# Optimization experiments

Measured on AMD Instinct MI355X. Metric: run time of the kernel, lower is better.

Reference implementation:

```python
import jax, jax.numpy as jnp
import numpy as np

SEQ = 4096
D_EMB = 2048
D_HEAD = 128
SCALE = 0.02


def setup_inputs() -> dict:
    key = jax.random.key(0)
    kx, kq, kk, kv, ko = jax.random.split(key, 5)
    x = jax.random.normal(kx, (SEQ, D_EMB), dtype=jnp.float32)
    W_Q = jax.random.normal(kq, (D_EMB, D_EMB), dtype=jnp.float32) * SCALE
    W_K = jax.random.normal(kk, (D_EMB, D_EMB), dtype=jnp.float32) * SCALE
    W_V = jax.random.normal(kv, (D_EMB, D_EMB), dtype=jnp.float32) * SCALE
    W_O = jax.random.normal(ko, (D_EMB, D_EMB), dtype=jnp.float32) * SCALE
    b_Q = jnp.zeros((D_EMB,), dtype=jnp.float32)
    b_K = jnp.zeros((D_EMB,), dtype=jnp.float32)
    b_V = jnp.zeros((D_EMB,), dtype=jnp.float32)
    b_O = jnp.zeros((D_EMB,), dtype=jnp.float32)
    return {"x": x, "W_Q": W_Q, "W_K": W_K, "W_V": W_V, "W_O": W_O,
            "b_Q": b_Q, "b_K": b_K, "b_V": b_V, "b_O": b_O, "d_head": D_HEAD}


def reference(x, W_Q, W_K, W_V, W_O, b_Q, b_K, b_V, b_O, d_head):
    # x: [S, D]
    q = x @ W_Q + b_Q  # [S, D]
    k = x @ W_K + b_K
    v = x @ W_V + b_V
    scores = (q @ k.T) / jnp.sqrt(jnp.float32(d_head))  # [S, S]
    seq = scores.shape[0]
    causal = jnp.tril(jnp.ones((seq, seq), dtype=bool))
    scores = jnp.where(causal, scores, -jnp.inf)
    weights = jax.nn.softmax(scores, axis=-1)  # [S, S]
    attn_out = weights @ v  # [S, D]
    return attn_out @ W_O + b_O
```

## Files before the change

### kernel.cpp

```cpp
#include <hip/hip_runtime.h>
#include <hip/hip_fp16.h>

typedef _Float16 f16;
typedef _Float16 f16x8 __attribute__((ext_vector_type(8)));
typedef _Float16 f16x4 __attribute__((ext_vector_type(4)));
typedef float    f32x4 __attribute__((ext_vector_type(4)));

#define SEQ      4096
#define DEMB     2048
#define SCALE_QK 0.08838834764831845f

#define GAS __attribute__((address_space(1)))
#define LAS __attribute__((address_space(3)))

__device__ __forceinline__ void load_lds16(const f16* g, f16* l) {
    __builtin_amdgcn_global_load_lds((const GAS void*)g, (LAS void*)l, 16, 0, 0);
}

__device__ __forceinline__ f16x8 ldsr(const f16* base, int byteoff) {
    byteoff ^= (byteoff >> 3) & 0x70;
    return *(const f16x8*)((const char*)base + byteoff);
}

__device__ __forceinline__ void stage_half(const f16* __restrict__ src, int ldk,
                                           f16* ldsdst, int tid) {
#pragma unroll
    for (int s = 0; s < 2; ++s) {
        const int o   = s * 8192 + tid * 16;
        const int osw = o ^ ((o >> 3) & 0x70);
        load_lds16(src + (size_t)(osw >> 7) * ldk + ((osw & 127) >> 1),
                   ldsdst + (s * 8192 + (tid >> 6) * 1024) / 2);
    }
}

template <int MODE>
__device__ __forceinline__ void gemm_core(
        const f16* __restrict__ A, int lda, const f16* __restrict__ BT, int ldb,
        void* __restrict__ outp, int ldo, const float* __restrict__ bias,
        int bm, int bn, int NI, int kt0, float scale, f16* lds, int roff) {
    const int m0 = bm * 256, n0 = bn * 256;

    const int tid  = threadIdx.x;
    const int lane = tid & 63;
    const int wr   = (tid >> 6) >> 2;
    const int wc   = (tid >> 6) & 3;
    const int fr   = lane & 15;
    const int kb   = (lane >> 4) * 16;

    const f16* Abase = A + (size_t)m0 * lda + kt0 * 64;
    const f16* Bbase = BT + (size_t)n0 * ldb + kt0 * 64;

#define STG(buf, isB, half, t) \
    stage_half((isB) ? (Bbase + (size_t)((half) * 128) * ldb + (t) * 64) \
                     : (Abase + (size_t)((half) * 128) * lda + (t) * 64), \
               (isB) ? ldb : lda, \
               lds + (buf) * 32768 + (isB) * 16384 + (half) * 8192, tid)

    f32x4 acc[8][4] = {};
    f16x8 af[8], bf0[4], bf1[4];

#define READ_A(Mh, buf) { \
    const f16* bb = lds + (buf) * 32768; \
    _Pragma("unroll") for (int m = 0; m < 4; ++m) \
    _Pragma("unroll") for (int ks = 0; ks < 2; ++ks) \
        af[m * 2 + ks] = ldsr(bb, ((Mh) * 128 + wr * 64 + m * 16 + fr) * 128 + ks * 64 + kb); }

#define READ_B(Nh, buf, dst) { \
    const f16* bb = lds + (buf) * 32768 + 16384; \
    _Pragma("unroll") for (int n = 0; n < 2; ++n) \
    _Pragma("unroll") for (int ks = 0; ks < 2; ++ks) \
        dst[n * 2 + ks] = ldsr(bb, ((Nh) * 128 + wc * 32 + n * 16 + fr) * 128 + ks * 64 + kb); }

#define MFMA_PH(Mh, Nh, bfx) { \
    __builtin_amdgcn_s_setprio(1); \
    _Pragma("unroll") for (int m = 0; m < 4; ++m) \
    _Pragma("unroll") for (int n = 0; n < 2; ++n) \
    _Pragma("unroll") for (int ks = 0; ks < 2; ++ks) \
        acc[(Mh) * 4 + m][(Nh) * 2 + n] = __builtin_amdgcn_mfma_f32_16x16x32_f16( \
            af[m * 2 + ks], bfx[n * 2 + ks], acc[(Mh) * 4 + m][(Nh) * 2 + n], 0, 0, 0); \
    __builtin_amdgcn_s_setprio(0); }

#define BAR   asm volatile("s_barrier" ::: "memory")
#define VM6   asm volatile("s_waitcnt vmcnt(6)" ::: "memory")
#define VM0   asm volatile("s_waitcnt vmcnt(0)" ::: "memory")

    STG(0, 0, 0, 0); STG(0, 1, 0, 0); STG(0, 1, 1, 0); STG(0, 0, 1, 0);
    STG(1, 0, 0, 1); STG(1, 1, 0, 1); STG(1, 1, 1, 1);
    VM6; BAR;

    for (int i = 0; i < NI; ++i) {
        const int t0 = 2 * i;
        const bool more = (i + 1 < NI);
        READ_A(0, 0); READ_B(0, 0, bf0);
        STG(1, 0, 1, t0 + 1);
        BAR; MFMA_PH(0, 0, bf0); BAR;
        READ_B(1, 0, bf1);
        if (more) STG(0, 0, 0, t0 + 2);
        BAR; MFMA_PH(0, 1, bf1); BAR;
        READ_A(1, 0);
        if (more) STG(0, 1, 0, t0 + 2);
        BAR; MFMA_PH(1, 0, bf0); BAR;
        if (more) { STG(0, 1, 1, t0 + 2); VM6; } else { VM0; }
        BAR; MFMA_PH(1, 1, bf1); BAR;
        READ_A(0, 1); READ_B(0, 1, bf0);
        if (more) STG(0, 0, 1, t0 + 2);
        BAR; MFMA_PH(0, 0, bf0); BAR;
        READ_B(1, 1, bf1);
        if (more) STG(1, 0, 0, t0 + 3);
        BAR; MFMA_PH(0, 1, bf1); BAR;
        READ_A(1, 1);
        if (more) STG(1, 1, 0, t0 + 3);
        BAR; MFMA_PH(1, 0, bf0); BAR;
        if (more) STG(1, 1, 1, t0 + 3);
        VM6;
        BAR; MFMA_PH(1, 1, bf1); BAR;
    }

    const int rq = (lane >> 4) * 4;
#pragma unroll
    for (int mi = 0; mi < 8; ++mi) {
        const int row = m0 + (mi >> 2) * 128 + wr * 64 + (mi & 3) * 16 + rq;
#pragma unroll
        for (int ni = 0; ni < 4; ++ni) {
            const int col = n0 + (ni >> 1) * 128 + wc * 32 + (ni & 1) * 16 + fr;
            if (MODE == 0) {
                f16* o = (f16*)outp;
                const float bv = bias[col];
#pragma unroll
                for (int r = 0; r < 4; ++r)
                    o[(size_t)(row + r) * ldo + col] = (f16)(acc[mi][ni][r] + bv);
            } else if (MODE == 1) {
                f16* o = (f16*)outp;
                f16x4 v;
#pragma unroll
                for (int r = 0; r < 4; ++r) v[r] = (f16)acc[mi][ni][r];
                *(f16x4*)&o[(size_t)col * ldo + row] = v;
            } else if (MODE == 2) {
                float* o = (float*)outp;
                if (bias) {
                    const float bv = bias[col];
#pragma unroll
                    for (int r = 0; r < 4; ++r)
                        o[(size_t)(row + r) * ldo + col] = acc[mi][ni][r] + bv;
                } else {
#pragma unroll
                    for (int r = 0; r < 4; ++r)
                        o[(size_t)(row - roff + r) * ldo + col] = acc[mi][ni][r];
                }
            } else {
                f16* o = (f16*)outp;
#pragma unroll
                for (int r = 0; r < 4; ++r)
                    o[(size_t)(row + r) * ldo + col] = (f16)(acc[mi][ni][r] * scale);
            }
        }
    }
#undef STG
#undef READ_A
#undef READ_B
#undef MFMA_PH
#undef BAR
#undef VM6
#undef VM0
}

__global__ __launch_bounds__(256) void k_prep(
        const float* __restrict__ x, const float* __restrict__ WV,
        const float* __restrict__ WQ, const float* __restrict__ WK,
        const float* __restrict__ WO,
        const float* __restrict__ bQ, const float* __restrict__ bK,
        const float* __restrict__ bO,
        f16* __restrict__ x16, f16* __restrict__ wv16,
        f16* __restrict__ wqkt, f16* __restrict__ wot,
        float* __restrict__ bqk, float* __restrict__ bc) {
    __shared__ f16 tile[64][72];
    const int bid = blockIdx.x;
    if (bid < 12288) {
        const bool isX = bid < 8192;
        const float* src = isX ? x : WV;
        f16* dst = isX ? x16 : wv16;
        const int i = (isX ? bid : bid - 8192) * 1024 + threadIdx.x * 4;
        float4 v = *(const float4*)&src[i];
        f16x4 o; o[0] = (f16)v.x; o[1] = (f16)v.y; o[2] = (f16)v.z; o[3] = (f16)v.w;
        *(f16x4*)&dst[i] = o;
        return;
    }
    if (bid < 12292) {
        const int i = (bid - 12288) * 1024 + threadIdx.x * 4;
        float4 v = (i < 2048) ? *(const float4*)&bQ[i]
                              : *(const float4*)&bK[i - 2048];
        *(float4*)&bqk[i] = v;
        return;
    }
    if (bid < 12294) {
        const int i = (bid - 12292) * 1024 + threadIdx.x * 4;
        *(float4*)&bc[i] = *(const float4*)&bO[i];
        return;
    }
    const int b = bid - 12294;
    const int z = b >> 10;
    const int rem = b & 1023;
    const float* in = z == 0 ? WQ : z == 1 ? WK : WO;
    f16* out = z == 0 ? wqkt : z == 1 ? wqkt + (size_t)DEMB * DEMB : wot;
    const int c0 = (rem & 31) * 64, r0 = (rem >> 5) * 64;
    const int tx = threadIdx.x & 63, ty = threadIdx.x >> 6;
    for (int rr = ty; rr < 64; rr += 4)
        tile[tx][rr] = (f16)in[(size_t)(r0 + rr) * DEMB + c0 + tx];
    __syncthreads();
    for (int cc = ty; cc < 64; cc += 4)
        out[(size_t)(c0 + cc) * DEMB + r0 + tx] = tile[cc][tx];
}

__global__ __launch_bounds__(512, 2)
void k_mix1(const f16* __restrict__ x16, const f16* __restrict__ wqkt,
            f16* __restrict__ qk16, const float* __restrict__ bqk,
            const f16* __restrict__ wv16, const f16* __restrict__ wot,
            f16* __restrict__ wvoT, const float* __restrict__ WO,
            const float* __restrict__ bV, float* __restrict__ bc) {
    __shared__ f16 lds[65536];
    const int bid = blockIdx.x;
    if (bid < 128) {
        gemm_core<0>(x16, DEMB, wqkt, DEMB, qk16, 2 * DEMB, bqk,
                     bid >> 4, bid & 15, 16, 0, 1.f, lds, 0);
    } else if (bid < 192) {
        const int w = bid - 128;
        gemm_core<1>(wv16, DEMB, wot, DEMB, wvoT, DEMB, nullptr,
                     w >> 3, w & 7, 16, 0, 1.f, lds, 0);
    } else {
        const int b  = bid - 192;
        const int j0 = (b & 7) * 256;
        const int i0 = (b >> 3) * 256 + (threadIdx.x >> 8) * 128;
        const int jj = threadIdx.x & 255;
        float acc = 0.f;
        for (int i = i0; i < i0 + 128; ++i)
            acc += bV[i] * WO[(size_t)i * DEMB + j0 + jj];
        atomicAdd(&bc[j0 + jj], acc);
    }
}

__global__ __launch_bounds__(512, 2)
void k_mix2(const f16* __restrict__ x16, const f16* __restrict__ wqkt,
            f16* __restrict__ qk16, const float* __restrict__ bqk,
            const f16* __restrict__ wvoT, f16* __restrict__ vwT) {
    __shared__ f16 lds[65536];
    const int bid = blockIdx.x;
    if (bid < 128) {
        gemm_core<0>(x16, DEMB, wqkt, DEMB, qk16, 2 * DEMB, bqk,
                     8 + (bid >> 4), bid & 15, 16, 0, 1.f, lds, 0);
    } else {
        const int b = bid - 128;
        const int bmv = ((b & 7) << 1) | ((b >> 3) & 1);
        const int bnv = b >> 4;
        gemm_core<1>(x16, DEMB, wvoT, DEMB, vwT, SEQ, nullptr,
                     bmv, bnv, 16, 0, 1.f, lds, 0);
    }
}

__global__ __launch_bounds__(512, 2)
void k_scores(const f16* __restrict__ qk16, f16* __restrict__ sb) {
    __shared__ f16 lds[65536];
    const int l = blockIdx.x;
    const int bid = (l & 7) * 17 + (l >> 3);
    int bm = (int)((sqrtf(8.f * bid + 1.f) - 1.f) * 0.5f);
    while ((bm + 1) * (bm + 2) / 2 <= bid) ++bm;
    while (bm * (bm + 1) / 2 > bid) --bm;
    const int bn = bid - bm * (bm + 1) / 2;
    gemm_core<3>(qk16, 2 * DEMB, qk16 + DEMB, 2 * DEMB, sb, SEQ, nullptr,
                 bm, bn, 16, 0, SCALE_QK, lds, 0);
}

__global__ __launch_bounds__(256) void k_softmax(f16* __restrict__ sb) {
    __shared__ f16 srow[SEQ];
    __shared__ float red[8];
    const int i  = blockIdx.x;
    const int L  = i + 1;
    const int Lp = ((i >> 8) + 1) << 8;
    f16* row = sb + (size_t)i * SEQ;
    const int t = threadIdx.x;

    float mx = -3.0e38f;
    for (int j0 = t * 8; j0 < Lp; j0 += 2048) {
        f16x8 v = *(const f16x8*)&row[j0];
        *(f16x8*)&srow[j0] = v;
#pragma unroll
        for (int u = 0; u < 8; ++u)
            if (j0 + u < L) mx = fmaxf(mx, (float)v[u]);
    }
#pragma unroll
    for (int o = 32; o > 0; o >>= 1) mx = fmaxf(mx, __shfl_xor(mx, o));
    if ((t & 63) == 0) red[t >> 6] = mx;
    __syncthreads();
    mx = fmaxf(fmaxf(red[0], red[1]), fmaxf(red[2], red[3]));

    float sm = 0.f;
    for (int j0 = t * 8; j0 < Lp; j0 += 2048) {
        f16x8 v = *(const f16x8*)&srow[j0];
        f16x8 e;
#pragma unroll
        for (int u = 0; u < 8; ++u) {
            const float ev = (j0 + u < L) ? __expf((float)v[u] - mx) : 0.f;
            sm += ev;
            e[u] = (f16)ev;
        }
        *(f16x8*)&srow[j0] = e;
    }
#pragma unroll
    for (int o = 32; o > 0; o >>= 1) sm += __shfl_xor(sm, o);
    if ((t & 63) == 0) red[4 + (t >> 6)] = sm;
    __syncthreads();
    const float inv = 1.f / (red[4] + red[5] + red[6] + red[7]);

    for (int j0 = t * 8; j0 < Lp; j0 += 2048) {
        f16x8 e = *(const f16x8*)&srow[j0];
        f16x8 wv;
#pragma unroll
        for (int u = 0; u < 8; ++u)
            wv[u] = (f16)((float)e[u] * inv);
        *(f16x8*)&row[j0] = wv;
    }
}

__global__ __launch_bounds__(512, 2)
void k_pvw(const f16* __restrict__ sb, const f16* __restrict__ vwT,
           float* __restrict__ out, const float* __restrict__ bc,
           float* __restrict__ part1, float* __restrict__ part2) {
    __shared__ f16 lds[65536];
    static const short BMt[32]  = {0,1,2,3,4, 5,5, 6,6, 7,7, 8,8, 9,9, 10,10,
                                   11,11,11, 12,12,12, 13,13,13, 14,14,14,
                                   15,15,15};
    static const short KT0t[32] = {0,0,0,0,0, 0,12, 0,14, 0,16, 0,18, 0,20,
                                   0,22, 0,16,32, 0,18,36, 0,20,38, 0,20,40,
                                   0,22,44};
    static const short NIt[32]  = {2,4,6,8,10, 6,6, 7,7, 8,8, 9,9, 10,10,
                                   11,11, 8,8,8, 9,9,8, 10,9,9, 10,10,10,
                                   11,11,10};
    static const short ORDt[32] = {0,0,0,0,0, 0,1, 0,1, 0,1, 0,1, 0,1, 0,1,
                                   0,1,2, 0,1,2, 0,1,2, 0,1,2, 0,1,2};
    const int bn = blockIdx.x, e = blockIdx.y;
    const int bm = BMt[e], kt0 = KT0t[e], ni = NIt[e], ord = ORDt[e];
    float* op = ord == 0 ? out : ord == 1 ? part1 : part2;
    const int roff = ord == 1 ? 1280 : 2816;
    gemm_core<2>(sb, SEQ, vwT, SEQ, op, DEMB, ord == 0 ? bc : nullptr,
                 bm, bn, ni, kt0, 1.f, lds, roff);
}

__global__ __launch_bounds__(256) void k_reduce(
        float* __restrict__ out, const float* __restrict__ part1,
        const float* __restrict__ part2) {
    const int idx = (blockIdx.x * 256 + threadIdx.x) * 4;
    float4 o = *(float4*)&out[(size_t)1280 * DEMB + idx];
    float4 p = *(const float4*)&part1[idx];
    o.x += p.x; o.y += p.y; o.z += p.z; o.w += p.w;
    if (idx >= 1536 * DEMB) {
        float4 q = *(const float4*)&part2[idx - 1536 * DEMB];
        o.x += q.x; o.y += q.y; o.z += q.z; o.w += q.w;
    }
    *(float4*)&out[(size_t)1280 * DEMB + idx] = o;
}

extern "C" void kernel_launch(void* const* d_in, const int* in_sizes, int n_in,
                              void* d_out, int out_size, void* d_ws, size_t ws_size,
                              hipStream_t stream) {
    const float* x  = (const float*)d_in[0];
    const float* WQ = (const float*)d_in[1];
    const float* WK = (const float*)d_in[2];
    const float* WV = (const float*)d_in[3];
    const float* WO = (const float*)d_in[4];
    const float* bQ = (const float*)d_in[5];
    const float* bK = (const float*)d_in[6];
    const float* bV = (const float*)d_in[7];
    const float* bO = (const float*)d_in[8];
    float* out = (float*)d_out;

    char* w = (char*)d_ws;
    f16* qk16 = (f16*)w; w += (size_t)SEQ * 2 * DEMB * 2;
    f16* sb   = (f16*)w; w += (size_t)SEQ * SEQ * 2;
    f16* x16  = (f16*)w; w += (size_t)SEQ * DEMB * 2;
    f16* wqkt = (f16*)w; w += (size_t)2 * DEMB * DEMB * 2;
    f16* wv16 = (f16*)w; w += (size_t)DEMB * DEMB * 2;
    f16* wot  = (f16*)w; w += (size_t)DEMB * DEMB * 2;
    f16* wvoT = (f16*)w; w += (size_t)DEMB * DEMB * 2;
    float* bqk = (float*)w; w += 2 * DEMB * 4;
    float* bc  = (float*)w; w += DEMB * 4 + 4096;
    f16* vwT = wv16;
    float* part1 = (float*)qk16;
    float* part2 = (float*)wqkt;

    k_prep<<<15366, 256, 0, stream>>>(x, WV, WQ, WK, WO, bQ, bK, bO,
                                      x16, wv16, wqkt, wot, bqk, bc);

    k_mix1<<<256, 512, 0, stream>>>(x16, wqkt, qk16, bqk, wv16, wot, wvoT,
                                    WO, bV, bc);

    k_mix2<<<256, 512, 0, stream>>>(x16, wqkt, qk16, bqk, wvoT, vwT);

    k_scores<<<136, 512, 0, stream>>>(qk16, sb);

    k_softmax<<<SEQ, 256, 0, stream>>>(sb);

    k_pvw<<<dim3(8, 32), 512, 0, stream>>>(sb, vwT, out, bc, part1, part2);

    k_reduce<<<5632, 256, 0, stream>>>(out, part1, part2);
}
```

Measured before the change: 278.6 us.

## Merge GEMM MFMA phases into four per iteration and regroup staging loads

Restructures the GEMM main loop from eight barrier-separated MFMA phases into four larger phases. Each phase now covers both N-halves, reading both B fragments up front. Staging loads are grouped three at a time and the vmcnt wait threshold drops from 6 to 3 to match. The aim is to halve the barrier count and give each MFMA burst more work, at the cost of more live B-fragment registers and less interleaving of global loads with compute.

```diff
diff --git a/kernel.cpp b/kernel.cpp
--- a/kernel.cpp
+++ b/kernel.cpp
@@ -71,49 +71,51 @@
     _Pragma("unroll") for (int ks = 0; ks < 2; ++ks) \
         dst[n * 2 + ks] = ldsr(bb, ((Nh) * 128 + wc * 32 + n * 16 + fr) * 128 + ks * 64 + kb); }
 
-#define MFMA_PH(Mh, Nh, bfx) { \
+#define MFMA2(Mh) { \
     __builtin_amdgcn_s_setprio(1); \
     _Pragma("unroll") for (int m = 0; m < 4; ++m) \
     _Pragma("unroll") for (int n = 0; n < 2; ++n) \
     _Pragma("unroll") for (int ks = 0; ks < 2; ++ks) \
-        acc[(Mh) * 4 + m][(Nh) * 2 + n] = __builtin_amdgcn_mfma_f32_16x16x32_f16( \
-            af[m * 2 + ks], bfx[n * 2 + ks], acc[(Mh) * 4 + m][(Nh) * 2 + n], 0, 0, 0); \
+        acc[(Mh) * 4 + m][n] = __builtin_amdgcn_mfma_f32_16x16x32_f16( \
+            af[m * 2 + ks], bf0[n * 2 + ks], acc[(Mh) * 4 + m][n], 0, 0, 0); \
+    _Pragma("unroll") for (int m = 0; m < 4; ++m) \
+    _Pragma("unroll") for (int n = 0; n < 2; ++n) \
+    _Pragma("unroll") for (int ks = 0; ks < 2; ++ks) \
+        acc[(Mh) * 4 + m][2 + n] = __builtin_amdgcn_mfma_f32_16x16x32_f16( \
+            af[m * 2 + ks], bf1[n * 2 + ks], acc[(Mh) * 4 + m][2 + n], 0, 0, 0); \
     __builtin_amdgcn_s_setprio(0); }
 
 #define BAR   asm volatile("s_barrier" ::: "memory")
-#define VM6   asm volatile("s_waitcnt vmcnt(6)" ::: "memory")
+#define VM3   asm volatile("s_waitcnt vmcnt(3)" ::: "memory")
 #define VM0   asm volatile("s_waitcnt vmcnt(0)" ::: "memory")
 
     STG(0, 0, 0, 0); STG(0, 1, 0, 0); STG(0, 1, 1, 0); STG(0, 0, 1, 0);
     STG(1, 0, 0, 1); STG(1, 1, 0, 1); STG(1, 1, 1, 1);
-    VM6; BAR;
+    VM3; BAR;
 
     for (int i = 0; i < NI; ++i) {
         const int t0 = 2 * i;
         const bool more = (i + 1 < NI);
-        READ_A(0, 0); READ_B(0, 0, bf0);
+        READ_A(0, 0); READ_B(0, 0, bf0); READ_B(1, 0, bf1);
         STG(1, 0, 1, t0 + 1);
-        BAR; MFMA_PH(0, 0, bf0); BAR;
-        READ_B(1, 0, bf1);
-        if (more) STG(0, 0, 0, t0 + 2);
-        BAR; MFMA_PH(0, 1, bf1); BAR;
+        BAR; MFMA2(0); BAR;
         READ_A(1, 0);
-        if (more) STG(0, 1, 0, t0 + 2);
-        BAR; MFMA_PH(1, 0, bf0); BAR;
-        if (more) { STG(0, 1, 1, t0 + 2); VM6; } else { VM0; }
-        BAR; MFMA_PH(1, 1, bf1); BAR;
-        READ_A(0, 1); READ_B(0, 1, bf0);
+        if (more) {
+            STG(0, 0, 0, t0 + 2); STG(0, 1, 0, t0 + 2); STG(0, 1, 1, t0 + 2);
+            VM3;
+        } else {
+            VM0;
+        }
+        BAR; MFMA2(1); BAR;
+        READ_A(0, 1); READ_B(0, 1, bf0); READ_B(1, 1, bf1);
         if (more) STG(0, 0, 1, t0 + 2);
-        BAR; MFMA_PH(0, 0, bf0); BAR;
-        READ_B(1, 1, bf1);
-        if (more) STG(1, 0, 0, t0 + 3);
-        BAR; MFMA_PH(0, 1, bf1); BAR;
+        BAR; MFMA2(0); BAR;
         READ_A(1, 1);
-        if (more) STG(1, 1, 0, t0 + 3);
-        BAR; MFMA_PH(1, 0, bf0); BAR;
-        if (more) STG(1, 1, 1, t0 + 3);
-        VM6;
-        BAR; MFMA_PH(1, 1, bf1); BAR;
+        if (more) {
+            STG(1, 0, 0, t0 + 3); STG(1, 1, 0, t0 + 3); STG(1, 1, 1, t0 + 3);
+        }
+        VM3;
+        BAR; MFMA2(1); BAR;
     }
 
     const int rq = (lane >> 4) * 4;
@@ -158,9 +160,9 @@
 #undef STG
 #undef READ_A
 #undef READ_B
-#undef MFMA_PH
+#undef MFMA2
 #undef BAR
-#undef VM6
+#undef VM3
 #undef VM0
 }
 
```

New measurement: 309.8 us. 1.11x slower.
